# Performance work log

Measured on AMD Instinct MI355X. Metric: run time of the kernel, lower is better.

The kernel has to match this reference:

```python
import jax, jax.numpy as jnp
import numpy as np

NEG_INF = -1e20
SLOPE = 0.2  # LeakyReLU slope ('relu' init arg)
N_NODES, N_FEAT, N_HID, N_HEADS = 23, 1, 2, 2


def setup_inputs() -> dict:
    key = jax.random.key(0)
    ks = jax.random.split(key, 12)
    B = 16384
    node_attr_matrix = jax.random.normal(ks[0], (B, N_NODES, N_FEAT), dtype=jnp.float32)
    adjacency_matrix = jax.random.randint(ks[1], (B, N_NODES, N_NODES), 0, 2, dtype=jnp.int32)

    def xavier(k, shape, gain=1.414):
        fan_in, fan_out = shape[0], shape[1]
        lim = gain * np.sqrt(6.0 / (fan_in + fan_out))
        return jax.random.uniform(k, shape, jnp.float32, -lim, lim)

    return {
        "node_attr_matrix": node_attr_matrix,
        "adjacency_matrix": adjacency_matrix,
        "W0": xavier(ks[2], (N_FEAT, N_HID)),
        "a0": xavier(ks[3], (2 * N_HID, 1)),
        "W1": xavier(ks[4], (N_FEAT, N_HID)),
        "a1": xavier(ks[5], (2 * N_HID, 1)),
        "fc1_w": xavier(ks[6], (N_NODES * N_HID * N_HEADS, 128), gain=1.0),
        "fc1_b": jnp.zeros((128,), jnp.float32),
        "pre_w": xavier(ks[7], (128, 16), gain=1.0),
        "pre_b": jnp.zeros((16,), jnp.float32),
        "predict_w": xavier(ks[8], (16, 1), gain=1.0),
        "predict_b": jnp.zeros((1,), jnp.float32),
        "getvar_w": xavier(ks[9], (16, 1), gain=1.0),
        "getvar_b": jnp.zeros((1,), jnp.float32),
    }


def gat_layer(x, adj, W, a):
    # x: [B,N,Fin], adj: [B,N,N]
    h = jnp.matmul(x, W)  # [B,N,F]
    F_out = W.shape[1]
    # e[i,j] = leakyrelu(h_i . a[:F] + h_j . a[F:])  (avoids O(N^2*2F) concat)
    f1 = jnp.matmul(h, a[:F_out])            # [B,N,1]
    f2 = jnp.matmul(h, a[F_out:])            # [B,N,1]
    e = jax.nn.leaky_relu(f1 + jnp.swapaxes(f2, 1, 2), SLOPE)  # [B,N,N]
    e = jnp.where(adj > 0, e, NEG_INF)
    att = jax.nn.softmax(e, axis=1)          # NOTE: dim=1 as in the torch code
    h_prime = jnp.matmul(att, h)             # [B,N,F]
    return jax.nn.gelu(h_prime, approximate=False)  # concat=True branch


def reference(node_attr_matrix, adjacency_matrix, W0, a0, W1, a1,
              fc1_w, fc1_b, pre_w, pre_b, predict_w, predict_b,
              getvar_w, getvar_b):
    adj = adjacency_matrix.astype(jnp.float32)
    x = node_attr_matrix.astype(jnp.float32)[:, :N_NODES, :]
    # two attention heads, concatenated on feature dim
    x = jnp.concatenate([gat_layer(x, adj, W0, a0),
                         gat_layer(x, adj, W1, a1)], axis=2)  # [B,23,4]
    x = x.reshape(x.shape[0], -1)  # [B,92]
    xc = jax.nn.relu(x @ fc1_w + fc1_b)                 # fc1 (dropout off, eval)
    xp = jax.nn.gelu(xc @ pre_w + pre_b, approximate=False)  # pre
    y = jax.nn.relu(xp @ predict_w + predict_b)         # predict
    var = xp @ getvar_w + getvar_b                      # get_var
    return (y, var, xc)
```

## Files before the change

### kernel.cpp

```cpp
#include <hip/hip_runtime.h>
#include <hip/hip_bf16.h>

#define NN 23
#define BLK 256
#define SPB 16
#define WST 104
#define XST 136

typedef __attribute__((ext_vector_type(8))) short bf16x8;
typedef __attribute__((ext_vector_type(4))) float f32x4;

__device__ __forceinline__ unsigned short f2b(float f) {
    union { __hip_bfloat16 h; unsigned short u; } c; c.h = __float2bfloat16(f); return c.u;
}
__device__ __forceinline__ float geluf(float v) {
    return 0.5f * v * (1.0f + erff(v * 0.70710678118654752f));
}

__global__ __launch_bounds__(BLK, 4) void gat_fused(
    const float* __restrict__ xattr, const int* __restrict__ adj,
    const float* __restrict__ W0,   const float* __restrict__ a0,
    const float* __restrict__ W1,   const float* __restrict__ a1,
    const float* __restrict__ fc1w, const float* __restrict__ fc1b,
    const float* __restrict__ prew, const float* __restrict__ preb,
    const float* __restrict__ predw, const float* __restrict__ predb,
    const float* __restrict__ varw,  const float* __restrict__ varb,
    float* __restrict__ outy, float* __restrict__ outv, float* __restrict__ outxc)
{
    __shared__ unsigned short s_w1t[128 * WST];
    __shared__ unsigned short s_feat[SPB * WST];
    __shared__ unsigned short s_xc[SPB * XST];
    __shared__ unsigned short s_pwt[16 * XST];
    __shared__ float s_fc1b[128];
    __shared__ float s_aux[64];

    const int tid = threadIdx.x;

    for (int i = tid; i < 92 * 128; i += BLK) {
        const int m = i >> 7, n = i & 127;
        s_w1t[n * WST + m] = f2b(fc1w[i]);
    }
    for (int i = tid; i < 256; i += BLK) {
        const int n = i >> 1, u = i & 1;
        *(unsigned*)&s_w1t[n * WST + 92 + 2 * u] = 0u;
    }
    if (tid < 32) {
        const int r = tid >> 1, u = tid & 1;
        *(unsigned*)&s_feat[r * WST + 92 + 2 * u] = 0u;
    }
    for (int i = tid; i < 2048; i += BLK) {
        const int k = i >> 4, t = i & 15;
        s_pwt[t * XST + k] = f2b(prew[i]);
    }
    if (tid < 128) s_fc1b[tid] = fc1b[tid];
    if (tid < 16) {
        s_aux[12 + tid] = preb[tid];
        s_aux[28 + tid] = predw[tid];
        s_aux[44 + tid] = varw[tid];
    }
    if (tid == 0) {
        s_aux[0] = W0[0]; s_aux[1] = W0[1];
        s_aux[2] = a0[0]; s_aux[3] = a0[1]; s_aux[4] = a0[2]; s_aux[5] = a0[3];
        s_aux[6] = W1[0]; s_aux[7] = W1[1];
        s_aux[8] = a1[0]; s_aux[9] = a1[1]; s_aux[10] = a1[2]; s_aux[11] = a1[3];
        s_aux[60] = predb[0]; s_aux[61] = varb[0];
    }
    __syncthreads();

    const int group = tid >> 5;
    const int l     = tid & 31;

    #pragma unroll 1
    for (int rnd = 0; rnd < 2; ++rnd) {
        const int sl = group * 2 + rnd;
        const int s  = blockIdx.x * SPB + sl;

        float xl = 0.0f;
        if (l < NN) xl = xattr[s * NN + l];
        float xv[NN];
        #pragma unroll
        for (int i = 0; i < NN; ++i) xv[i] = __shfl(xl, i, 32);

        unsigned cm = 0u;
        if (l < NN) {
            const int* ar = adj + (size_t)s * (NN * NN);
            #pragma unroll
            for (int i = 0; i < NN; ++i) cm |= (ar[i * NN + l] != 0) ? (1u << i) : 0u;
        }
        unsigned rm = 0u;
        #pragma unroll
        for (int i = 0; i < NN; ++i) {
            unsigned long long bal = __ballot((cm >> i) & 1u);
            unsigned half = (unsigned)(bal >> (tid & 32));
            rm = (l == i) ? half : rm;
        }
        unsigned em;
        {
            unsigned long long bal = __ballot(cm == 0u);
            em = ((unsigned)(bal >> (tid & 32))) & 0x7FFFFFu;
        }
        float sbase = 0.0f;
        #pragma unroll
        for (int j = 0; j < NN; ++j) sbase += ((em >> j) & 1u) ? xv[j] : 0.0f;
        sbase *= (1.0f / 23.0f);

        float fmine[4];
        #pragma unroll
        for (int h = 0; h < 2; ++h) {
            const float w0 = s_aux[h * 6 + 0], w1 = s_aux[h * 6 + 1];
            const float c1 = w0 * s_aux[h * 6 + 2] + w1 * s_aux[h * 6 + 3];
            const float c2 = w0 * s_aux[h * 6 + 4] + w1 * s_aux[h * 6 + 5];

            const float f2l = xl * c2;
            float dcol = 0.0f;
            #pragma unroll
            for (int i = 0; i < NN; ++i) {
                float e = fmaf(xv[i], c1, f2l);
                e = fmaxf(e, 0.2f * e);
                float t = ((cm >> i) & 1u) ? 1.0f : 0.0f;
                dcol = fmaf(__expf(e), t, dcol);
            }
            const float scl = (cm == 0u) ? 0.0f : __fdividef(xl, dcol);

            float sclv[NN];
            #pragma unroll
            for (int j = 0; j < NN; ++j) sclv[j] = __shfl(scl, j, 32);

            const float f1 = xl * c1;
            float sown = sbase;
            #pragma unroll
            for (int j = 0; j < NN; ++j) {
                float e = fmaf(xv[j], c2, f1);
                e = fmaxf(e, 0.2f * e);
                float t = ((rm >> j) & 1u) ? sclv[j] : 0.0f;
                sown = fmaf(__expf(e), t, sown);
            }
            fmine[h * 2 + 0] = geluf(w0 * sown);
            fmine[h * 2 + 1] = geluf(w1 * sown);
        }

        if (l < NN) {
            unsigned lo = (unsigned)f2b(fmine[0]) | ((unsigned)f2b(fmine[1]) << 16);
            unsigned hi = (unsigned)f2b(fmine[2]) | ((unsigned)f2b(fmine[3]) << 16);
            *(uint2*)&s_feat[sl * WST + 4 * l] = make_uint2(lo, hi);
        }
    }
    __syncthreads();

    {
        const int wave = tid >> 6;
        const int lane = tid & 63;
        const int q    = lane >> 4;
        const int c16  = lane & 15;

        f32x4 acc0 = {0.f, 0.f, 0.f, 0.f};
        f32x4 acc1 = {0.f, 0.f, 0.f, 0.f};
        const int n0 = 32 * wave + c16;
        const int n1 = n0 + 16;
        #pragma unroll
        for (int t = 0; t < 3; ++t) {
            const bf16x8 a  = *(const bf16x8*)&s_feat[c16 * WST + 32 * t + 8 * q];
            const bf16x8 b0 = *(const bf16x8*)&s_w1t[n0 * WST + 32 * t + 8 * q];
            const bf16x8 b1 = *(const bf16x8*)&s_w1t[n1 * WST + 32 * t + 8 * q];
            acc0 = __builtin_amdgcn_mfma_f32_16x16x32_bf16(a, b0, acc0, 0, 0, 0);
            acc1 = __builtin_amdgcn_mfma_f32_16x16x32_bf16(a, b1, acc1, 0, 0, 0);
        }
        const float bia0 = s_fc1b[n0], bia1 = s_fc1b[n1];
        const size_t gbase = (size_t)blockIdx.x * SPB * 128;
        #pragma unroll
        for (int r = 0; r < 4; ++r) {
            const int srow = 4 * q + r;
            const float v0 = fmaxf(acc0[r] + bia0, 0.0f);
            const float v1 = fmaxf(acc1[r] + bia1, 0.0f);
            outxc[gbase + (size_t)srow * 128 + n0] = v0;
            outxc[gbase + (size_t)srow * 128 + n1] = v1;
            s_xc[srow * XST + n0] = f2b(v0);
            s_xc[srow * XST + n1] = f2b(v1);
        }
    }
    __syncthreads();

    if (tid < 64) {
        const int q   = tid >> 4;
        const int c16 = tid & 15;
        f32x4 acc = {0.f, 0.f, 0.f, 0.f};
        #pragma unroll
        for (int t = 0; t < 4; ++t) {
            const bf16x8 a = *(const bf16x8*)&s_xc[c16 * XST + 32 * t + 8 * q];
            const bf16x8 b = *(const bf16x8*)&s_pwt[c16 * XST + 32 * t + 8 * q];
            acc = __builtin_amdgcn_mfma_f32_16x16x32_bf16(a, b, acc, 0, 0, 0);
        }
        const float pb = s_aux[12 + c16], pw = s_aux[28 + c16], vw = s_aux[44 + c16];
        float yp[4], vp[4];
        #pragma unroll
        for (int r = 0; r < 4; ++r) {
            const float g = geluf(acc[r] + pb);
            yp[r] = g * pw;
            vp[r] = g * vw;
        }
        #pragma unroll
        for (int m = 1; m < 16; m <<= 1) {
            #pragma unroll
            for (int r = 0; r < 4; ++r) {
                yp[r] += __shfl_xor(yp[r], m, 64);
                vp[r] += __shfl_xor(vp[r], m, 64);
            }
        }
        if (c16 == 0) {
            const int sb = blockIdx.x * SPB + 4 * q;
            #pragma unroll
            for (int r = 0; r < 4; ++r) {
                outy[sb + r] = fmaxf(yp[r] + s_aux[60], 0.0f);
                outv[sb + r] = vp[r] + s_aux[61];
            }
        }
    }
}

extern "C" void kernel_launch(void* const* d_in, const int* in_sizes, int n_in,
                              void* d_out, int out_size, void* d_ws, size_t ws_size,
                              hipStream_t stream) {
    const float* xattr = (const float*)d_in[0];
    const int*   adjp  = (const int*)d_in[1];

    const int B = in_sizes[0] / NN;
    float* o = (float*)d_out;
    float* outy  = o;
    float* outv  = o + B;
    float* outxc = o + 2 * (size_t)B;

    gat_fused<<<dim3(B / SPB), dim3(BLK), 0, stream>>>(
        xattr, adjp,
        (const float*)d_in[2], (const float*)d_in[3],
        (const float*)d_in[4], (const float*)d_in[5],
        (const float*)d_in[6], (const float*)d_in[7],
        (const float*)d_in[8], (const float*)d_in[9],
        (const float*)d_in[10], (const float*)d_in[11],
        (const float*)d_in[12], (const float*)d_in[13],
        outy, outv, outxc);
}
```

Measured before the change: 119.8 us.

## Pre-transpose weights to bf16 in a prep kernel, read from global

A small prep kernel converts and transposes fc1 and pre weights to bf16 in workspace each call. The main kernel drops its per-block staging of those weights into LDS and loads the MFMA B operands straight from global (L2-cached) memory. This removes a large per-block LDS fill and sync cost and reduces LDS use, allowing launch bounds to rise to 8 blocks per SM. It adds a second launch and uncoalesced-ish global loads in the MFMA loop.

Result: slower. 174.5 us (+45.6%).

```diff
diff --git a/kernel.cpp b/kernel.cpp
--- a/kernel.cpp
+++ b/kernel.cpp
@@ -6,6 +6,8 @@
 #define SPB 16
 #define WST 104
 #define XST 136
+#define W1TK 96
+#define PWTK 128
 
 typedef __attribute__((ext_vector_type(8))) short bf16x8;
 typedef __attribute__((ext_vector_type(4))) float f32x4;
@@ -17,54 +19,57 @@
     return 0.5f * v * (1.0f + erff(v * 0.70710678118654752f));
 }
 
-__global__ __launch_bounds__(BLK, 4) void gat_fused(
+__global__ __launch_bounds__(256) void prep(const float* __restrict__ fc1w,
+                                            const float* __restrict__ prew,
+                                            unsigned short* __restrict__ w1t,
+                                            unsigned short* __restrict__ pwt) {
+    const int tid = blockIdx.x * 256 + threadIdx.x;
+    const int NT = gridDim.x * 256;
+    for (int i = tid; i < 128 * W1TK; i += NT) {
+        const int n = i / W1TK, k = i - n * W1TK;
+        w1t[i] = (k < 92) ? f2b(fc1w[k * 128 + n]) : (unsigned short)0;
+    }
+    for (int j = tid; j < 16 * PWTK; j += NT) {
+        const int t = j >> 7, k = j & 127;
+        pwt[j] = f2b(prew[k * 16 + t]);
+    }
+}
+
+__global__ __launch_bounds__(BLK, 8) void gat_fused(
     const float* __restrict__ xattr, const int* __restrict__ adj,
     const float* __restrict__ W0,   const float* __restrict__ a0,
     const float* __restrict__ W1,   const float* __restrict__ a1,
-    const float* __restrict__ fc1w, const float* __restrict__ fc1b,
-    const float* __restrict__ prew, const float* __restrict__ preb,
+    const unsigned short* __restrict__ w1t, const float* __restrict__ fc1b,
+    const unsigned short* __restrict__ pwt, const float* __restrict__ preb,
     const float* __restrict__ predw, const float* __restrict__ predb,
     const float* __restrict__ varw,  const float* __restrict__ varb,
     float* __restrict__ outy, float* __restrict__ outv, float* __restrict__ outxc)
 {
-    __shared__ unsigned short s_w1t[128 * WST];
     __shared__ unsigned short s_feat[SPB * WST];
     __shared__ unsigned short s_xc[SPB * XST];
-    __shared__ unsigned short s_pwt[16 * XST];
     __shared__ float s_fc1b[128];
     __shared__ float s_aux[64];
 
     const int tid = threadIdx.x;
 
-    for (int i = tid; i < 92 * 128; i += BLK) {
-        const int m = i >> 7, n = i & 127;
-        s_w1t[n * WST + m] = f2b(fc1w[i]);
-    }
-    for (int i = tid; i < 256; i += BLK) {
-        const int n = i >> 1, u = i & 1;
-        *(unsigned*)&s_w1t[n * WST + 92 + 2 * u] = 0u;
-    }
-    if (tid < 32) {
-        const int r = tid >> 1, u = tid & 1;
-        *(unsigned*)&s_feat[r * WST + 92 + 2 * u] = 0u;
-    }
-    for (int i = tid; i < 2048; i += BLK) {
-        const int k = i >> 4, t = i & 15;
-        s_pwt[t * XST + k] = f2b(prew[i]);
-    }
     if (tid < 128) s_fc1b[tid] = fc1b[tid];
-    if (tid < 16) {
-        s_aux[12 + tid] = preb[tid];
-        s_aux[28 + tid] = predw[tid];
-        s_aux[44 + tid] = varw[tid];
-    }
-    if (tid == 0) {
+    if (tid >= 128 && tid < 144) {
+        const int t = tid - 128;
+        s_aux[12 + t] = preb[t];
+        s_aux[28 + t] = predw[t];
+        s_aux[44 + t] = varw[t];
+    }
+    if (tid == 144) {
         s_aux[0] = W0[0]; s_aux[1] = W0[1];
         s_aux[2] = a0[0]; s_aux[3] = a0[1]; s_aux[4] = a0[2]; s_aux[5] = a0[3];
         s_aux[6] = W1[0]; s_aux[7] = W1[1];
         s_aux[8] = a1[0]; s_aux[9] = a1[1]; s_aux[10] = a1[2]; s_aux[11] = a1[3];
         s_aux[60] = predb[0]; s_aux[61] = varb[0];
     }
+    if (tid >= 160 && tid < 192) {
+        const int r = (tid - 160) >> 1, u = tid & 1;
+        *(unsigned*)&s_feat[r * WST + 92 + 2 * u] = 0u;
+    }
     __syncthreads();
 
     const int group = tid >> 5;
@@ -160,8 +165,8 @@
         #pragma unroll
         for (int t = 0; t < 3; ++t) {
             const bf16x8 a  = *(const bf16x8*)&s_feat[c16 * WST + 32 * t + 8 * q];
-            const bf16x8 b0 = *(const bf16x8*)&s_w1t[n0 * WST + 32 * t + 8 * q];
-            const bf16x8 b1 = *(const bf16x8*)&s_w1t[n1 * WST + 32 * t + 8 * q];
+            const bf16x8 b0 = *(const bf16x8*)&w1t[n0 * W1TK + 32 * t + 8 * q];
+            const bf16x8 b1 = *(const bf16x8*)&w1t[n1 * W1TK + 32 * t + 8 * q];
             acc0 = __builtin_amdgcn_mfma_f32_16x16x32_bf16(a, b0, acc0, 0, 0, 0);
             acc1 = __builtin_amdgcn_mfma_f32_16x16x32_bf16(a, b1, acc1, 0, 0, 0);
         }
@@ -187,7 +192,7 @@
         #pragma unroll
         for (int t = 0; t < 4; ++t) {
             const bf16x8 a = *(const bf16x8*)&s_xc[c16 * XST + 32 * t + 8 * q];
-            const bf16x8 b = *(const bf16x8*)&s_pwt[c16 * XST + 32 * t + 8 * q];
+            const bf16x8 b = *(const bf16x8*)&pwt[c16 * PWTK + 32 * t + 8 * q];
             acc = __builtin_amdgcn_mfma_f32_16x16x32_bf16(a, b, acc, 0, 0, 0);
         }
         const float pb = s_aux[12 + c16], pw = s_aux[28 + c16], vw = s_aux[44 + c16];
@@ -229,12 +234,18 @@
     float* outv  = o + B;
     float* outxc = o + 2 * (size_t)B;
 
+    unsigned short* w1t = (unsigned short*)d_ws;
+    unsigned short* pwt = (unsigned short*)((char*)d_ws + 24576);
+
+    prep<<<dim3(16), dim3(256), 0, stream>>>(
+        (const float*)d_in[6], (const float*)d_in[8], w1t, pwt);
+
     gat_fused<<<dim3(B / SPB), dim3(BLK), 0, stream>>>(
         xattr, adjp,
         (const float*)d_in[2], (const float*)d_in[3],
         (const float*)d_in[4], (const float*)d_in[5],
-        (const float*)d_in[6], (const float*)d_in[7],
-        (const float*)d_in[8], (const float*)d_in[9],
+        w1t, (const float*)d_in[7],
+        pwt, (const float*)d_in[9],
         (const float*)d_in[10], (const float*)d_in[11],
         (const float*)d_in[12], (const float*)d_in[13],
         outy, outv, outxc);
```
